# Kernel optimization log

Hardware: AMD Instinct MI355X
Metric: run time of the kernel (lower is better)

Reference implementation:

```python
import jax, jax.numpy as jnp
import numpy as np
import math

N_HEAD = 4
NORM_GROUPS = 16
EPS = 1e-5


def setup_inputs() -> dict:
    key = jax.random.key(0)
    ks = jax.random.split(key, 4)
    B, C, H, W = 2, 256, 64, 64
    return {
        "input": jax.random.normal(ks[0], (B, C, H, W), dtype=jnp.float32),
        "gn_weight": jnp.ones((C,), dtype=jnp.float32),
        "gn_bias": jnp.zeros((C,), dtype=jnp.float32),
        # 1x1 convs are plain channel matmuls: weight [out_ch, in_ch]
        "qkv_weight": jax.random.normal(ks[1], (3 * C, C), dtype=jnp.float32) / math.sqrt(C),
        "out_weight": jax.random.normal(ks[2], (C, C), dtype=jnp.float32) / math.sqrt(C),
        "out_bias": jnp.zeros((C,), dtype=jnp.float32),
    }


def _group_norm(x, weight, bias):
    B, C, H, W = x.shape
    g = x.reshape(B, NORM_GROUPS, C // NORM_GROUPS, H, W)
    mu = g.mean(axis=(2, 3, 4), keepdims=True)
    var = g.var(axis=(2, 3, 4), keepdims=True)
    g = (g - mu) * jax.lax.rsqrt(var + EPS)
    return g.reshape(B, C, H, W) * weight[:, None, None] + bias[:, None, None]


def reference(input, gn_weight, gn_bias, qkv_weight, out_weight, out_bias):
    B, C, H, W = input.shape
    head_dim = C // N_HEAD
    x = _group_norm(input, gn_weight, gn_bias)
    # 1x1 conv (no bias) -> [B, 3C, H, W] -> [B, n_head, 3*head_dim, H, W]
    qkv = jnp.einsum('bchw,oc->bohw', x, qkv_weight)
    qkv = qkv.reshape(B, N_HEAD, 3 * head_dim, H, W)
    q, k, v = jnp.split(qkv, 3, axis=2)
    # full spatial attention; note: scale is sqrt(channel), as in the source
    attn = jnp.einsum('bnchw,bncyx->bnhwyx', q, k) / math.sqrt(C)
    attn = jax.nn.softmax(attn.reshape(B, N_HEAD, H, W, H * W), axis=-1)
    attn = attn.reshape(B, N_HEAD, H, W, H, W)
    out = jnp.einsum('bnhwyx,bncyx->bnchw', attn, v).reshape(B, C, H, W)
    out = jnp.einsum('bchw,oc->bohw', out, out_weight) + out_bias[:, None, None]
    return out + input
```

## Files before the change

kernel.cpp:

```cpp
#include <hip/hip_runtime.h>

typedef __bf16        bf16x8 __attribute__((ext_vector_type(8)));
typedef float         f32x4  __attribute__((ext_vector_type(4)));
typedef unsigned short u16x4 __attribute__((ext_vector_type(4)));
typedef unsigned short u16x8 __attribute__((ext_vector_type(8)));
typedef unsigned int  u32x4  __attribute__((ext_vector_type(4)));

#define MFMA16(a,b,c) __builtin_amdgcn_mfma_f32_16x16x32_bf16((a),(b),(c),0,0,0)

static __device__ __forceinline__ unsigned short f2bf(float f) {
  unsigned int u = __builtin_bit_cast(unsigned int, f);
  u += 0x7fffu + ((u >> 16) & 1u);
  return (unsigned short)(u >> 16);
}
static __device__ __forceinline__ unsigned int pk2rne(float a, float b) {
  return (unsigned int)f2bf(a) | ((unsigned int)f2bf(b) << 16);
}
static __device__ __forceinline__ unsigned int pkrn(float a, float b) {
#if __has_builtin(__builtin_amdgcn_cvt_pk_bf16_f32)
  auto r = __builtin_amdgcn_cvt_pk_bf16_f32(a, b);
  return __builtin_bit_cast(unsigned int, r);
#else
  return pk2rne(a, b);
#endif
}
static __device__ __forceinline__ bf16x8 as_bf(u32x4 v) {
  return __builtin_bit_cast(bf16x8, v);
}

#define SDIM 4096
#define CDIM 256
#define NHEAD 4
#define HDIM 64
#define NBATCH 2

__global__ __launch_bounds__(256) void k_prep(const float* __restrict__ x,
                                              const float* __restrict__ wq,
                                              const float* __restrict__ wo,
                                              unsigned short* __restrict__ wqf,
                                              unsigned short* __restrict__ wof,
                                              float2* __restrict__ Sp) {
  int j = blockIdx.x, i = threadIdx.x;
  if (j < 256) {
    const float* p = x + (size_t)(j >> 3) * 65536 + (size_t)(j & 7) * 8192;
    float s = 0.f, sq = 0.f;
#pragma unroll
    for (int r = 0; r < 8; ++r) {
      float4 v = *(const float4*)(p + (r * 256 + i) * 4);
      s  += v.x + v.y + v.z + v.w;
      sq += v.x * v.x + v.y * v.y + v.z * v.z + v.w * v.w;
    }
    __shared__ float rs[256], rq[256];
    rs[i] = s; rq[i] = sq;
    __syncthreads();
    for (int off = 128; off > 0; off >>= 1) {
      if (i < off) { rs[i] += rs[i + off]; rq[i] += rq[i + off]; }
      __syncthreads();
    }
    if (i == 0) Sp[j] = make_float2(rs[0], rq[0]);
  } else {
    int t = (j - 256) * 256 + i;
#pragma unroll
    for (int u = 0; u < 2; ++u) {
      int G = t * 2 + u;
      const float* src; unsigned short* dst;
      if (G < 24576) {
        int tile = G >> 6, l = G & 63;
        src = wq + (size_t)((tile >> 3) * 16 + (l & 15)) * 256 + (tile & 7) * 32 + (l >> 4) * 8;
        dst = wqf + (size_t)G * 8;
      } else {
        int G2 = G - 24576, tile = G2 >> 6, l = G2 & 63;
        src = wo + (size_t)((tile >> 3) * 16 + (l & 15)) * 256 + (tile & 7) * 32 + (l >> 4) * 8;
        dst = wof + (size_t)G2 * 8;
      }
      float4 v0 = *(const float4*)src, v1 = *(const float4*)(src + 4);
      u16x8 r;
      r[0] = f2bf(v0.x); r[1] = f2bf(v0.y); r[2] = f2bf(v0.z); r[3] = f2bf(v0.w);
      r[4] = f2bf(v1.x); r[5] = f2bf(v1.y); r[6] = f2bf(v1.z); r[7] = f2bf(v1.w);
      *(u16x8*)dst = r;
    }
  }
}

__global__ __launch_bounds__(256) void k_gn_apply(const float* __restrict__ x,
                                                  const float2* __restrict__ Sp,
                                                  const float* __restrict__ gnw,
                                                  const float* __restrict__ gnb,
                                                  unsigned short* __restrict__ Xf) {
  __shared__ __attribute__((aligned(16))) unsigned short sT[64 * 268];
  __shared__ float2 sStat[16];
  int b = blockIdx.y, s0 = blockIdx.x * 64;
  int i = threadIdx.x, lane = i & 63, w = i >> 6;
  if (i < 16) {
    float s = 0.f, sq = 0.f;
#pragma unroll
    for (int u = 0; u < 8; ++u) {
      float2 v = Sp[(b * 16 + i) * 8 + u];
      s += v.x; sq += v.y;
    }
    float mean = s * (1.f / 65536.f);
    float var  = sq * (1.f / 65536.f) - mean * mean;
    sStat[i] = make_float2(mean, rsqrtf(var + 1e-5f));
  }
  __syncthreads();
#pragma unroll 4
  for (int r = 0; r < 64; ++r) {
    int c = r * 4 + w;
    float v = x[((size_t)(b * CDIM + c)) * SDIM + s0 + lane];
    float2 st = sStat[c >> 4];
    float nv = (v - st.x) * st.y * gnw[c] + gnb[c];
    sT[lane * 268 + c] = f2bf(nv);
  }
  __syncthreads();
  int l = i & 63, fr = i >> 6;
#pragma unroll
  for (int g = 0; g < 8; ++g) {
    int tile = fr * 8 + g, st = tile >> 3, kc = tile & 7;
    const unsigned short* src = &sT[(st * 16 + (l & 15)) * 268 + kc * 32 + (l >> 4) * 8];
    u16x4 lo = *(const u16x4*)src, hi = *(const u16x4*)(src + 4);
    unsigned short* dst = Xf + (((size_t)(b * 256 + (s0 >> 4) + st) * 8 + kc) * 64 + l) * 8;
    *(u16x4*)dst = lo;
    *(u16x4*)(dst + 4) = hi;
  }
}

__global__ __launch_bounds__(256) void k_qkv(const unsigned short* __restrict__ Wf,
                                             const unsigned short* __restrict__ Xf,
                                             unsigned short* __restrict__ Qf,
                                             unsigned short* __restrict__ Kf,
                                             unsigned short* __restrict__ Vf) {
  __shared__ __attribute__((aligned(16))) unsigned short sB[64 * 68];
  int b = blockIdx.z, s0 = blockIdx.y * 64, o0 = blockIdx.x * 64;
  int i = threadIdx.x, lane = i & 63, w = i >> 6;
  int quad = lane >> 4, m = lane & 15;
  int ot = blockIdx.x * 4 + w;
  int stg = s0 >> 4;

  f32x4 acc[4] = {};
#pragma unroll
  for (int kc = 0; kc < 8; ++kc) {
    bf16x8 aW = as_bf(*(const u32x4*)(Wf + (((size_t)ot * 8 + kc) * 64 + lane) * 8));
#pragma unroll
    for (int st = 0; st < 4; ++st) {
      bf16x8 bX = as_bf(*(const u32x4*)(Xf + ((((size_t)b * 256 + stg + st) * 8 + kc) * 64 + lane) * 8));
      acc[st] = MFMA16(aW, bX, acc[st]);
    }
  }

  int sec = (o0 >> 6) % 3;
  int h   = o0 / 192;
  int bh  = b * NHEAD + h;
  float qs = (sec == 0) ? 0.09016844f : 1.0f;
#pragma unroll
  for (int st = 0; st < 4; ++st) {
    uint2 pk = make_uint2(pk2rne(acc[st][0] * qs, acc[st][1] * qs),
                          pk2rne(acc[st][2] * qs, acc[st][3] * qs));
    *(uint2*)&sB[(st * 16 + m) * 68 + w * 16 + quad * 4] = pk;
  }
  __syncthreads();
  int lp = i & 63, qp = lp >> 4, mp = lp & 15, t = i >> 6;
  if (sec < 2) {
    unsigned short* base = (sec == 0) ? Qf : Kf;
#pragma unroll
    for (int ks = 0; ks < 2; ++ks) {
      const unsigned short* src = &sB[(t * 16 + mp) * 68 + ks * 32 + qp * 8];
      u16x4 lo = *(const u16x4*)src;
      u16x4 hi = *(const u16x4*)(src + 4);
      unsigned short* dst = base + ((((size_t)bh * 256 + (s0 >> 4) + t) * 2 + ks) * 64 + lp) * 8;
      *(u16x4*)dst = lo;
      *(u16x4*)(dst + 4) = hi;
    }
  } else {
    int kt32l = t >> 1, dts = (t & 1) * 2;
#pragma unroll
    for (int dd = 0; dd < 2; ++dd) {
      int dt = dts + dd;
      u16x8 v;
#pragma unroll
      for (int jj = 0; jj < 8; ++jj)
        v[jj] = sB[(kt32l * 32 + qp * 8 + jj) * 68 + dt * 16 + mp];
      unsigned short* dst = Vf + ((((size_t)bh * 128 + (s0 >> 5) + kt32l) * 4 + dt) * 64 + lp) * 8;
      *(u16x8*)dst = v;
    }
  }
}

template <int KS>
__global__ __launch_bounds__(256, 4) void k_attn(const unsigned short* __restrict__ Qf,
                                                 const unsigned short* __restrict__ Kf,
                                                 const unsigned short* __restrict__ Vf,
                                                 unsigned short* __restrict__ Opb,
                                                 float* __restrict__ Lp) {
  __shared__ __attribute__((aligned(16))) unsigned short smem[128 * 72];
  int bh = blockIdx.y, kk = blockIdx.z;
  int i = threadIdx.x, lane = i & 63, w = i >> 6;
  int quad = lane >> 4, m = lane & 15;
  constexpr int ITERS = SDIM / KS / 32;
  unsigned short* sP = smem + w * 1280;

  bf16x8 bq[2][2];
#pragma unroll
  for (int qt = 0; qt < 2; ++qt)
#pragma unroll
    for (int ks = 0; ks < 2; ++ks)
      bq[qt][ks] = as_bf(*(const u32x4*)(Qf +
        ((((size_t)bh * 256 + (blockIdx.x * 8 + w * 2 + qt)) * 2 + ks) * 64 + lane) * 8));

  f32x4 oacc[2][4] = {};
  float li[2] = {0.f, 0.f};

  for (int it = 0; it < ITERS; ++it) {
    bf16x8 av[4];
    int kb32 = kk * ITERS + it;
#pragma unroll
    for (int dt = 0; dt < 4; ++dt)
      av[dt] = as_bf(*(const u32x4*)(Vf +
        ((((size_t)bh * 128 + kb32) * 4 + dt) * 64 + lane) * 8));

    bf16x8 ak[2][2];
    int kb16 = kk * (ITERS * 2) + it * 2;
#pragma unroll
    for (int ky = 0; ky < 2; ++ky)
#pragma unroll
      for (int ks = 0; ks < 2; ++ks)
        ak[ky][ks] = as_bf(*(const u32x4*)(Kf +
          ((((size_t)bh * 256 + kb16 + ky) * 2 + ks) * 64 + lane) * 8));

#pragma unroll
    for (int qt = 0; qt < 2; ++qt) {
      f32x4 sc0 = {-18.f, -18.f, -18.f, -18.f};
      f32x4 sc1 = sc0;
      sc0 = MFMA16(ak[0][0], bq[qt][0], sc0);
      sc0 = MFMA16(ak[0][1], bq[qt][1], sc0);
      sc1 = MFMA16(ak[1][0], bq[qt][0], sc1);
      sc1 = MFMA16(ak[1][1], bq[qt][1], sc1);
      float p[8];
#pragma unroll
      for (int r = 0; r < 4; ++r) {
        p[r]     = __builtin_amdgcn_exp2f(sc0[r]);
        p[4 + r] = __builtin_amdgcn_exp2f(sc1[r]);
      }
      li[qt] += ((p[0] + p[1]) + (p[2] + p[3])) + ((p[4] + p[5]) + (p[6] + p[7]));
      int row = (qt * 16 + m) * 40;
      *(uint2*)&sP[row + quad * 4]      = make_uint2(pkrn(p[0], p[1]), pkrn(p[2], p[3]));
      *(uint2*)&sP[row + 16 + quad * 4] = make_uint2(pkrn(p[4], p[5]), pkrn(p[6], p[7]));
    }
#pragma unroll
    for (int qt = 0; qt < 2; ++qt) {
      bf16x8 bp = *(const bf16x8*)&sP[(qt * 16 + m) * 40 + quad * 8];
#pragma unroll
      for (int dt = 0; dt < 4; ++dt)
        oacc[qt][dt] = MFMA16(av[dt], bp, oacc[qt][dt]);
    }
  }

  size_t lg = (size_t)(kk * 8 + bh) * SDIM + blockIdx.x * 128 + w * 32;
#pragma unroll
  for (int qt = 0; qt < 2; ++qt) {
    li[qt] += __shfl_xor(li[qt], 16);
    li[qt] += __shfl_xor(li[qt], 32);
  }
  if (quad == 0) {
#pragma unroll
    for (int qt = 0; qt < 2; ++qt) Lp[lg + qt * 16 + m] = li[qt];
  }

  __syncthreads();
  unsigned short* ob = smem;
#pragma unroll
  for (int qt = 0; qt < 2; ++qt)
#pragma unroll
    for (int dt = 0; dt < 4; ++dt) {
      int ql = w * 32 + qt * 16 + m, d0 = dt * 16 + quad * 4;
      *(unsigned int*)&ob[ql * 72 + d0]     = pkrn(oacc[qt][dt][0], oacc[qt][dt][1]);
      *(unsigned int*)&ob[ql * 72 + d0 + 2] = pkrn(oacc[qt][dt][2], oacc[qt][dt][3]);
    }
  __syncthreads();
  int l = i & 63, sub = i >> 6, mp = l & 15, qp = l >> 4;
#pragma unroll
  for (int tt = 0; tt < 2; ++tt)
#pragma unroll
    for (int kc = 0; kc < 2; ++kc) {
      int t16l = sub * 2 + tt;
      u16x8 v = *(const u16x8*)&ob[(t16l * 16 + mp) * 72 + kc * 32 + qp * 8];
      size_t idx = ((((size_t)(kk * 8 + bh) * 256 + blockIdx.x * 8 + t16l) * 2 + kc) * 64 + l) * 8;
      *(u16x8*)(Opb + idx) = v;
    }
}

template <int KS>
__global__ __launch_bounds__(256, 4) void k_proj(const unsigned short* __restrict__ Wf,
                                                 const unsigned short* __restrict__ Opb,
                                                 const float* __restrict__ Lp,
                                                 const float* __restrict__ bias,
                                                 const float* __restrict__ resid,
                                                 float* __restrict__ out) {
  int b = blockIdx.z, s0 = blockIdx.y * 32, o0 = blockIdx.x * 64;
  int i = threadIdx.x, lane = i & 63, w = i >> 6;
  int quad = lane >> 4, m = lane & 15;
  int ot = blockIdx.x * 4 + w;
  int stg = s0 >> 4;

  f32x4 acc[4][2] = {};
#pragma unroll
  for (int kc = 0; kc < 8; ++kc) {
    bf16x8 aW = as_bf(*(const u32x4*)(Wf + (((size_t)ot * 8 + kc) * 64 + lane) * 8));
    int h = kc >> 1, kch = kc & 1;
#pragma unroll
    for (int kk = 0; kk < KS; ++kk) {
      size_t kb = (size_t)(kk * 8 + b * NHEAD + h);
#pragma unroll
      for (int st = 0; st < 2; ++st) {
        bf16x8 bX = as_bf(*(const u32x4*)(Opb +
          (((kb * 256 + stg + st) * 2 + kch) * 64 + lane) * 8));
        acc[h][st] = MFMA16(aW, bX, acc[h][st]);
      }
    }
  }

  float inv[4][2];
#pragma unroll
  for (int h = 0; h < 4; ++h)
#pragma unroll
    for (int st = 0; st < 2; ++st) {
      size_t base = (size_t)(b * NHEAD + h) * SDIM + s0 + st * 16 + m;
      float lsum = 0.f;
#pragma unroll
      for (int kk = 0; kk < KS; ++kk) lsum += Lp[base + (size_t)kk * 8 * SDIM];
      inv[h][st] = 1.f / lsum;
    }

#pragma unroll
  for (int st = 0; st < 2; ++st)
#pragma unroll
    for (int r = 0; r < 4; ++r) {
      int o = o0 + w * 16 + quad * 4 + r;
      int s = s0 + st * 16 + m;
      float v = acc[0][st][r] * inv[0][st] + acc[1][st][r] * inv[1][st] +
                acc[2][st][r] * inv[2][st] + acc[3][st][r] * inv[3][st];
      size_t idx = ((size_t)b * CDIM + o) * SDIM + s;
      out[idx] = v + bias[o] + resid[idx];
    }
}

extern "C" void kernel_launch(void* const* d_in, const int* in_sizes, int n_in,
                              void* d_out, int out_size, void* d_ws, size_t ws_size,
                              hipStream_t stream) {
  const float* input = (const float*)d_in[0];
  const float* gnw   = (const float*)d_in[1];
  const float* gnb   = (const float*)d_in[2];
  const float* wq    = (const float*)d_in[3];
  const float* wo    = (const float*)d_in[4];
  const float* ob    = (const float*)d_in[5];
  float* out = (float*)d_out;

  char* ws = (char*)d_ws;
  unsigned short* Xf  = (unsigned short*)(ws);
  unsigned short* Qf  = (unsigned short*)(ws + (4ull  << 20));
  unsigned short* Kf  = (unsigned short*)(ws + (8ull  << 20));
  unsigned short* Vf  = (unsigned short*)(ws + (12ull << 20));
  unsigned short* wqf = (unsigned short*)(ws + (20ull << 20));
  unsigned short* wof = (unsigned short*)(ws + (20ull << 20) + (1u << 19));
  float2* Sp          = (float2*)(ws + (20ull << 20) + (3u << 18));
  float* Lp           = (float*)(ws + (21ull << 20));
  unsigned short* Opb = (unsigned short*)(ws + (22ull << 20));

  k_prep<<<320, 256, 0, stream>>>(input, wq, wo, wqf, wof, Sp);
  k_gn_apply<<<dim3(64, NBATCH), 256, 0, stream>>>(input, Sp, gnw, gnb, Xf);
  k_qkv<<<dim3(12, 64, NBATCH), 256, 0, stream>>>(wqf, Xf, Qf, Kf, Vf);
  if (ws_size >= (54ull << 20)) {
    k_attn<8><<<dim3(32, NHEAD * NBATCH, 8), 256, 0, stream>>>(Qf, Kf, Vf, Opb, Lp);
    k_proj<8><<<dim3(4, 128, NBATCH), 256, 0, stream>>>(wof, Opb, Lp, ob, input, out);
  } else {
    k_attn<4><<<dim3(32, NHEAD * NBATCH, 4), 256, 0, stream>>>(Qf, Kf, Vf, Opb, Lp);
    k_proj<4><<<dim3(4, 128, NBATCH), 256, 0, stream>>>(wof, Opb, Lp, ob, input, out);
  }
}
```

Measured before the change: 175.6 us.

## Reduce split-K partials before projection and fix attention split to four

The projection kernel now sums the split-K attention partial outputs in fp32, scales them by the softmax normaliser, and stores the result as bf16 in shared memory. It then runs a single MFMA pass over the output weights, instead of one MFMA per split per head. This cuts the MFMA count in the projection by the split factor. The attention split is fixed at four rather than chosen as eight when the workspace is large enough. That lowers partial-output traffic but may reduce attention parallelism, and the extra bf16 rounding of the normalised sum changes numerics slightly.

```diff
diff --git a/kernel.cpp b/kernel.cpp
--- a/kernel.cpp
+++ b/kernel.cpp
@@ -27,12 +27,16 @@
 static __device__ __forceinline__ bf16x8 as_bf(u32x4 v) {
   return __builtin_bit_cast(bf16x8, v);
 }
+static __device__ __forceinline__ float bf2f(unsigned short u) {
+  return __builtin_bit_cast(float, ((unsigned int)u) << 16);
+}
 
 #define SDIM 4096
 #define CDIM 256
 #define NHEAD 4
 #define HDIM 64
 #define NBATCH 2
+#define KSPLIT 4
 
 __global__ __launch_bounds__(256) void k_prep(const float* __restrict__ x,
                                               const float* __restrict__ wq,
@@ -288,58 +292,69 @@
     }
 }
 
-template <int KS>
 __global__ __launch_bounds__(256, 4) void k_proj(const unsigned short* __restrict__ Wf,
                                                  const unsigned short* __restrict__ Opb,
                                                  const float* __restrict__ Lp,
                                                  const float* __restrict__ bias,
                                                  const float* __restrict__ resid,
                                                  float* __restrict__ out) {
-  int b = blockIdx.z, s0 = blockIdx.y * 32, o0 = blockIdx.x * 64;
+  __shared__ __attribute__((aligned(16))) unsigned short sPc[8 * 512];
+  __shared__ float sL[4][16];
+  int b = blockIdx.y, t16g = blockIdx.x, s0 = t16g * 16;
   int i = threadIdx.x, lane = i & 63, w = i >> 6;
   int quad = lane >> 4, m = lane & 15;
-  int ot = blockIdx.x * 4 + w;
-  int stg = s0 >> 4;
-
-  f32x4 acc[4][2] = {};
+
+  if (i < 64) {
+    int h = i >> 4, s = i & 15;
+    float lsum = 0.f;
+#pragma unroll
+    for (int kk = 0; kk < KSPLIT; ++kk)
+      lsum += Lp[(size_t)(kk * 8 + b * NHEAD + h) * SDIM + s0 + s];
+    sL[h][s] = 1.f / lsum;
+  }
+  __syncthreads();
+
+  int fr = i >> 6, l = i & 63;
+#pragma unroll
+  for (int f = 0; f < 2; ++f) {
+    int kcq = fr * 2 + f, h = kcq >> 1, kch = kcq & 1;
+    float o[8] = {};
+#pragma unroll
+    for (int kk = 0; kk < KSPLIT; ++kk) {
+      const unsigned short* p = Opb +
+        ((((size_t)(kk * 8 + b * NHEAD + h) * 256 + t16g) * 2 + kch) * 64 + l) * 8;
+      u16x8 v = *(const u16x8*)p;
+#pragma unroll
+      for (int e = 0; e < 8; ++e) o[e] += bf2f(v[e]);
+    }
+    float inv = sL[h][l & 15];
+    unsigned int dw[4];
+#pragma unroll
+    for (int e = 0; e < 4; ++e) dw[e] = pkrn(o[2 * e] * inv, o[2 * e + 1] * inv);
+    *(u32x4*)&sPc[kcq * 512 + l * 8] = u32x4{dw[0], dw[1], dw[2], dw[3]};
+  }
+  __syncthreads();
+
+  f32x4 acc[4] = {};
 #pragma unroll
   for (int kc = 0; kc < 8; ++kc) {
-    bf16x8 aW = as_bf(*(const u32x4*)(Wf + (((size_t)ot * 8 + kc) * 64 + lane) * 8));
-    int h = kc >> 1, kch = kc & 1;
-#pragma unroll
-    for (int kk = 0; kk < KS; ++kk) {
-      size_t kb = (size_t)(kk * 8 + b * NHEAD + h);
-#pragma unroll
-      for (int st = 0; st < 2; ++st) {
-        bf16x8 bX = as_bf(*(const u32x4*)(Opb +
-          (((kb * 256 + stg + st) * 2 + kch) * 64 + lane) * 8));
-        acc[h][st] = MFMA16(aW, bX, acc[h][st]);
-      }
-    }
-  }
-
-  float inv[4][2];
-#pragma unroll
-  for (int h = 0; h < 4; ++h)
-#pragma unroll
-    for (int st = 0; st < 2; ++st) {
-      size_t base = (size_t)(b * NHEAD + h) * SDIM + s0 + st * 16 + m;
-      float lsum = 0.f;
-#pragma unroll
-      for (int kk = 0; kk < KS; ++kk) lsum += Lp[base + (size_t)kk * 8 * SDIM];
-      inv[h][st] = 1.f / lsum;
-    }
-
-#pragma unroll
-  for (int st = 0; st < 2; ++st)
+    bf16x8 bP = *(const bf16x8*)&sPc[kc * 512 + lane * 8];
+#pragma unroll
+    for (int j = 0; j < 4; ++j) {
+      int ot = w * 4 + j;
+      bf16x8 aW = as_bf(*(const u32x4*)(Wf + (((size_t)ot * 8 + kc) * 64 + lane) * 8));
+      acc[j] = MFMA16(aW, bP, acc[j]);
+    }
+  }
+
+#pragma unroll
+  for (int j = 0; j < 4; ++j)
 #pragma unroll
     for (int r = 0; r < 4; ++r) {
-      int o = o0 + w * 16 + quad * 4 + r;
-      int s = s0 + st * 16 + m;
-      float v = acc[0][st][r] * inv[0][st] + acc[1][st][r] * inv[1][st] +
-                acc[2][st][r] * inv[2][st] + acc[3][st][r] * inv[3][st];
+      int o = (w * 4 + j) * 16 + quad * 4 + r;
+      int s = s0 + m;
       size_t idx = ((size_t)b * CDIM + o) * SDIM + s;
-      out[idx] = v + bias[o] + resid[idx];
+      out[idx] = acc[j][r] + bias[o] + resid[idx];
     }
 }
 
@@ -368,11 +383,6 @@
   k_prep<<<320, 256, 0, stream>>>(input, wq, wo, wqf, wof, Sp);
   k_gn_apply<<<dim3(64, NBATCH), 256, 0, stream>>>(input, Sp, gnw, gnb, Xf);
   k_qkv<<<dim3(12, 64, NBATCH), 256, 0, stream>>>(wqf, Xf, Qf, Kf, Vf);
-  if (ws_size >= (54ull << 20)) {
-    k_attn<8><<<dim3(32, NHEAD * NBATCH, 8), 256, 0, stream>>>(Qf, Kf, Vf, Opb, Lp);
-    k_proj<8><<<dim3(4, 128, NBATCH), 256, 0, stream>>>(wof, Opb, Lp, ob, input, out);
-  } else {
-    k_attn<4><<<dim3(32, NHEAD * NBATCH, 4), 256, 0, stream>>>(Qf, Kf, Vf, Opb, Lp);
-    k_proj<4><<<dim3(4, 128, NBATCH), 256, 0, stream>>>(wof, Opb, Lp, ob, input, out);
-  }
-}
+  k_attn<KSPLIT><<<dim3(32, NHEAD * NBATCH, KSPLIT), 256, 0, stream>>>(Qf, Kf, Vf, Opb, Lp);
+  k_proj<<<dim3(256, NBATCH), 256, 0, stream>>>(wof, Opb, Lp, ob, input, out);
+}
```

Measured after the change: 146.6 us. 16.5% less time.
